# Performance work log

Hardware: AMD Instinct MI355X
Metric: run time of the kernel (lower is better)

The kernel has to match this reference:

```python
import jax, jax.numpy as jnp
import numpy as np

EMB = 128
HID = 4 * 32  # 4*hidden_dim = 128
N_NODES = 100000
N_EDGES = 800000


def setup_inputs() -> dict:
    key = jax.random.key(0)
    k1, k2, k3, k4 = jax.random.split(key, 4)
    node_emb = jax.random.normal(k1, (N_NODES, EMB), dtype=jnp.float32)
    edge_index = jax.random.randint(k2, (2, N_EDGES), 0, N_NODES, dtype=jnp.int64)
    # xavier_uniform for Linear weights, zeros bias; LayerNorm gamma=1, beta=0
    lim1 = float(np.sqrt(6.0 / (2 * EMB + HID)))
    W1 = jax.random.uniform(k3, (2 * EMB, HID), minval=-lim1, maxval=lim1, dtype=jnp.float32)
    b1 = jnp.zeros((HID,), dtype=jnp.float32)
    ln_g = jnp.ones((HID,), dtype=jnp.float32)
    ln_b = jnp.zeros((HID,), dtype=jnp.float32)
    lim2 = float(np.sqrt(6.0 / (HID + 1)))
    W2 = jax.random.uniform(k4, (HID, 1), minval=-lim2, maxval=lim2, dtype=jnp.float32)
    b2 = jnp.zeros((1,), dtype=jnp.float32)
    return {"node_emb": node_emb, "edge_index": edge_index,
            "W1": W1, "b1": b1, "ln_g": ln_g, "ln_b": ln_b, "W2": W2, "b2": b2}


def reference(node_emb, edge_index, W1, b1, ln_g, ln_b, W2, b2):
    src, dst = edge_index[0], edge_index[1]
    # gather + concat: [E, 2*EMB]
    edge_emb = jnp.concatenate([node_emb[src], node_emb[dst]], axis=1)
    h = edge_emb @ W1 + b1  # [E, HID]
    # LayerNorm over last dim (eps=1e-5, torch default)
    mu = jnp.mean(h, axis=-1, keepdims=True)
    var = jnp.var(h, axis=-1, keepdims=True)
    h = (h - mu) * jax.lax.rsqrt(var + 1e-5) * ln_g + ln_b
    h = jax.nn.relu(h)  # Dropout is identity in eval mode
    w = jax.nn.sigmoid(h @ W2 + b2)  # [E, 1]
    w = jnp.nan_to_num(w, nan=0.5)
    return w
```

## Files before the change

### kernel.cpp

```cpp
#include <hip/hip_runtime.h>
#include <hip/hip_bf16.h>
#include <math.h>

#define EMB 128
#define HID 128
#define NCOL 256

typedef __attribute__((ext_vector_type(8))) short short8v;
typedef __attribute__((ext_vector_type(4))) float f32x4;

__device__ __forceinline__ unsigned short f2bf(float f) {
    union { float f; unsigned int u; } v; v.f = f;
    unsigned int r = (v.u + 0x7FFFu + ((v.u >> 16) & 1u)) >> 16;
    return (unsigned short)r;
}
__device__ __forceinline__ float bf2f(unsigned int u16) {
    return __uint_as_float(u16 << 16);
}

template<int CTRL>
__device__ __forceinline__ float dpp_add(float x) {
    int y = __builtin_amdgcn_update_dpp(0, __float_as_int(x), CTRL, 0xf, 0xf, true);
    return x + __int_as_float(y);
}
__device__ __forceinline__ float red16(float x) {
    x = dpp_add<0xB1>(x);
    x = dpp_add<0x4E>(x);
    x = dpp_add<0x141>(x);
    x = dpp_add<0x140>(x);
    return x;
}

__global__ __launch_bounds__(256) void w_prep(
    const float* __restrict__ W1, unsigned short* __restrict__ Wt)
{
    int idx = blockIdx.x * 256 + threadIdx.x;
    int c = idx >> 7;
    int k = idx & 127;
    float v = W1[(size_t)(k + ((c >> 7) << 7)) * HID + (c & 127)];
    Wt[idx] = f2bf(v);
}

__global__ __launch_bounds__(256) void proj_mfma(
    const float* __restrict__ A,
    const unsigned short* __restrict__ Wt,
    const float* __restrict__ b1,
    unsigned short* __restrict__ P,
    int N, int nTiles)
{
    const int w    = threadIdx.x >> 6;
    const int lane = threadIdx.x & 63;
    const int l16  = lane & 15;
    const int lk   = lane >> 4;

    short8v afrag[4][4];
#pragma unroll
    for (int cf = 0; cf < 4; ++cf)
#pragma unroll
        for (int ks = 0; ks < 4; ++ks) {
            int c = 64 * w + 16 * cf + l16;
            afrag[cf][ks] = *(const short8v*)(Wt + (size_t)c * EMB + 32 * ks + 8 * lk);
        }

    float4 b1v[4];
#pragma unroll
    for (int cf = 0; cf < 4; ++cf) {
        if (w < 2) b1v[cf] = *(const float4*)(b1 + 64 * w + 16 * cf + 4 * lk);
        else       b1v[cf] = make_float4(0.f, 0.f, 0.f, 0.f);
    }

    int t = blockIdx.x;
    if (t >= nTiles) return;

    float4 fbuf[8];
    {
        int node = t * 16 + l16;
        int nc   = node < N ? node : N - 1;
        const float* ap = A + (size_t)nc * EMB + 8 * lk;
#pragma unroll
        for (int ks = 0; ks < 4; ++ks) {
            fbuf[2 * ks]     = *(const float4*)(ap + 32 * ks);
            fbuf[2 * ks + 1] = *(const float4*)(ap + 32 * ks + 4);
        }
    }

    for (; t < nTiles; t += gridDim.x) {
        short8v bf[4];
#pragma unroll
        for (int ks = 0; ks < 4; ++ks) {
            float4 a0 = fbuf[2 * ks], a1 = fbuf[2 * ks + 1];
            short8v f = { (short)f2bf(a0.x), (short)f2bf(a0.y), (short)f2bf(a0.z), (short)f2bf(a0.w),
                          (short)f2bf(a1.x), (short)f2bf(a1.y), (short)f2bf(a1.z), (short)f2bf(a1.w) };
            bf[ks] = f;
        }

        int tn = t + gridDim.x;
        if (tn < nTiles) {
            int node = tn * 16 + l16;
            int nc   = node < N ? node : N - 1;
            const float* ap = A + (size_t)nc * EMB + 8 * lk;
#pragma unroll
            for (int ks = 0; ks < 4; ++ks) {
                fbuf[2 * ks]     = *(const float4*)(ap + 32 * ks);
                fbuf[2 * ks + 1] = *(const float4*)(ap + 32 * ks + 4);
            }
        }

        f32x4 acc[4];
#pragma unroll
        for (int cf = 0; cf < 4; ++cf) acc[cf] = (f32x4)0.0f;

#pragma unroll
        for (int ks = 0; ks < 4; ++ks)
#pragma unroll
            for (int cf = 0; cf < 4; ++cf)
                acc[cf] = __builtin_amdgcn_mfma_f32_16x16x32_bf16(
                    afrag[cf][ks], bf[ks], acc[cf], 0, 0, 0);

        int node = t * 16 + l16;
        if (node < N) {
            unsigned short* prow = P + (size_t)node * NCOL;
#pragma unroll
            for (int cf = 0; cf < 4; ++cf) {
                float v0 = acc[cf][0] + b1v[cf].x;
                float v1 = acc[cf][1] + b1v[cf].y;
                float v2 = acc[cf][2] + b1v[cf].z;
                float v3 = acc[cf][3] + b1v[cf].w;
                unsigned int u0 = (unsigned int)f2bf(v0) | ((unsigned int)f2bf(v1) << 16);
                unsigned int u1 = (unsigned int)f2bf(v2) | ((unsigned int)f2bf(v3) << 16);
                *(uint2*)(prow + 64 * w + 16 * cf + 4 * lk) = make_uint2(u0, u1);
            }
        }
    }
}

__global__ __launch_bounds__(256) void edge_kernel(
    const unsigned short* __restrict__ P,
    const int* __restrict__ ei,
    const float* __restrict__ lng,
    const float* __restrict__ lnb,
    const float* __restrict__ W2,
    const float* __restrict__ b2,
    float* __restrict__ out, int E)
{
    const int l16 = threadIdx.x & 15;
    const int c0  = l16 * 8;

    float vg[8], vbt[8], vw2[8];
#pragma unroll
    for (int i = 0; i < 8; i += 4) {
        *(float4*)&vg[i]  = *(const float4*)(lng + c0 + i);
        *(float4*)&vbt[i] = *(const float4*)(lnb + c0 + i);
        *(float4*)&vw2[i] = *(const float4*)(W2  + c0 + i);
    }
    const float bias2 = b2[0];

    int slot   = blockIdx.x * (blockDim.x >> 4) + (threadIdx.x >> 4);
    int nslots = gridDim.x * (blockDim.x >> 4);

    for (int e = slot; e < E; e += nslots) {
        int src = ei[e];
        int dst = ei[E + e];
        uint4 us = *(const uint4*)(P + (size_t)src * NCOL + c0);
        uint4 ud = *(const uint4*)(P + (size_t)dst * NCOL + HID + c0);

        float h[8];
        {
            unsigned int uu[4] = {us.x, us.y, us.z, us.w};
            unsigned int dd[4] = {ud.x, ud.y, ud.z, ud.w};
#pragma unroll
            for (int j = 0; j < 4; ++j) {
                h[2 * j]     = bf2f(uu[j] & 0xFFFFu) + bf2f(dd[j] & 0xFFFFu);
                h[2 * j + 1] = __uint_as_float(uu[j] & 0xFFFF0000u) +
                               __uint_as_float(dd[j] & 0xFFFF0000u);
            }
        }
        float s = 0.0f, sq = 0.0f;
#pragma unroll
        for (int i = 0; i < 8; ++i) {
            s += h[i];
            sq = fmaf(h[i], h[i], sq);
        }
        s  = red16(s);
        sq = red16(sq);

        float mu  = s * (1.0f / HID);
        float var = sq * (1.0f / HID) - mu * mu;
        float r   = rsqrtf(var + 1e-5f);
        float nmr = -mu * r;

        float z = 0.0f;
#pragma unroll
        for (int i = 0; i < 8; ++i) {
            float t = fmaf(h[i], r, nmr);
            float y = fmaf(t, vg[i], vbt[i]);
            y = fmaxf(y, 0.0f);
            z = fmaf(y, vw2[i], z);
        }
        z = red16(z);

        if (l16 == 0) {
            float zz = z + bias2;
            float wv = 1.0f / (1.0f + expf(-zz));
            if (wv != wv) wv = 0.5f;
            out[e] = wv;
        }
    }
}

__global__ __launch_bounds__(256) void fused_kernel(
    const float* __restrict__ X,
    const int* __restrict__ ei,
    const float* __restrict__ W1,
    const float* __restrict__ b1,
    const float* __restrict__ lng,
    const float* __restrict__ lnb,
    const float* __restrict__ W2,
    const float* __restrict__ b2,
    float* __restrict__ out, int E)
{
    const int lane = threadIdx.x & 31;
    const int c0   = lane * 4;
    const float4 vb1 = *(const float4*)(b1  + c0);
    const float4 vg  = *(const float4*)(lng + c0);
    const float4 vbt = *(const float4*)(lnb + c0);
    const float4 vw2 = *(const float4*)(W2  + c0);
    const float bias2 = b2[0];

    int slot   = blockIdx.x * (blockDim.x >> 5) + (threadIdx.x >> 5);
    int nslots = gridDim.x * (blockDim.x >> 5);

    for (int e = slot; e < E; e += nslots) {
        int src = ei[e];
        int dst = ei[E + e];
        const float* xs = X + (size_t)src * EMB;
        const float* xd = X + (size_t)dst * EMB;
        float h0 = vb1.x, h1 = vb1.y, h2 = vb1.z, h3 = vb1.w;
        for (int k = 0; k < EMB; ++k) {
            float a  = xs[k];
            float4 w = *(const float4*)(W1 + (size_t)k * HID + c0);
            h0 = fmaf(a, w.x, h0); h1 = fmaf(a, w.y, h1);
            h2 = fmaf(a, w.z, h2); h3 = fmaf(a, w.w, h3);
        }
        for (int k = 0; k < EMB; ++k) {
            float a  = xd[k];
            float4 w = *(const float4*)(W1 + (size_t)(EMB + k) * HID + c0);
            h0 = fmaf(a, w.x, h0); h1 = fmaf(a, w.y, h1);
            h2 = fmaf(a, w.z, h2); h3 = fmaf(a, w.w, h3);
        }
        float s  = h0 + h1 + h2 + h3;
        float sq = h0 * h0 + h1 * h1 + h2 * h2 + h3 * h3;
#pragma unroll
        for (int m = 16; m >= 1; m >>= 1) {
            s  += __shfl_xor(s,  m, 32);
            sq += __shfl_xor(sq, m, 32);
        }
        float mu  = s * (1.0f / HID);
        float var = sq * (1.0f / HID) - mu * mu;
        float r   = rsqrtf(var + 1e-5f);
        float y0 = fmaxf(fmaf((h0 - mu) * r, vg.x, vbt.x), 0.0f);
        float y1 = fmaxf(fmaf((h1 - mu) * r, vg.y, vbt.y), 0.0f);
        float y2 = fmaxf(fmaf((h2 - mu) * r, vg.z, vbt.z), 0.0f);
        float y3 = fmaxf(fmaf((h3 - mu) * r, vg.w, vbt.w), 0.0f);
        float z = y0 * vw2.x + y1 * vw2.y + y2 * vw2.z + y3 * vw2.w;
#pragma unroll
        for (int m = 16; m >= 1; m >>= 1) z += __shfl_xor(z, m, 32);
        if (lane == 0) {
            float zz = z + bias2;
            float wv = 1.0f / (1.0f + expf(-zz));
            if (wv != wv) wv = 0.5f;
            out[e] = wv;
        }
    }
}

extern "C" void kernel_launch(void* const* d_in, const int* in_sizes, int n_in,
                              void* d_out, int out_size, void* d_ws, size_t ws_size,
                              hipStream_t stream) {
    const float* node_emb = (const float*)d_in[0];
    const int*   ei       = (const int*)d_in[1];
    const float* W1       = (const float*)d_in[2];
    const float* b1       = (const float*)d_in[3];
    const float* lng      = (const float*)d_in[4];
    const float* lnb      = (const float*)d_in[5];
    const float* W2       = (const float*)d_in[6];
    const float* b2       = (const float*)d_in[7];
    float* out = (float*)d_out;

    const int N = in_sizes[0] / EMB;
    const int E = in_sizes[1] / 2;

    const size_t pBytes = (size_t)N * NCOL * sizeof(unsigned short);
    const size_t need   = pBytes + (size_t)NCOL * EMB * sizeof(unsigned short);

    if (ws_size >= need) {
        unsigned short* P  = (unsigned short*)d_ws;
        unsigned short* Wt = (unsigned short*)((char*)d_ws + pBytes);

        w_prep<<<(NCOL * EMB) / 256, 256, 0, stream>>>(W1, Wt);

        int nTiles = (N + 15) / 16;
        int gridP  = nTiles < 2048 ? nTiles : 2048;
        proj_mfma<<<gridP, 256, 0, stream>>>(node_emb, Wt, b1, P, N, nTiles);

        edge_kernel<<<4096, 256, 0, stream>>>(P, ei, lng, lnb, W2, b2, out, E);
    } else {
        fused_kernel<<<2048, 256, 0, stream>>>(node_emb, ei, W1, b1, lng, lnb,
                                               W2, b2, out, E);
    }
}
```

Baseline: 198.0 us.

## Stage 64-node tiles in swizzled LDS as bf16 for projection MFMA

The node projection kernel now loads a 64-node tile per block cooperatively with coalesced float4 reads. It converts the values to bf16 and stores them in an XOR-swizzled shared memory buffer, which every wave then reads from to feed MFMA for all four 16-node groups. Before, each wave separately loaded the same 16 nodes from global memory and prefetched through a grid-stride loop. The change removes four-fold redundant global reads and the strided access pattern, at the cost of 16KB of LDS per block, a barrier, and no overlap between loads of one tile and compute on the next.

```diff
diff --git a/kernel.cpp b/kernel.cpp
--- a/kernel.cpp
+++ b/kernel.cpp
@@ -48,10 +48,18 @@
     unsigned short* __restrict__ P,
     int N, int nTiles)
 {
-    const int w    = threadIdx.x >> 6;
-    const int lane = threadIdx.x & 63;
+    __shared__ unsigned short lds_bf[64 * 128];
+    char* ldsb = (char*)lds_bf;
+
+    const int tid  = threadIdx.x;
+    const int w    = tid >> 6;
+    const int lane = tid & 63;
     const int l16  = lane & 15;
     const int lk   = lane >> 4;
+
+    const int t = blockIdx.x;
+    if (t >= nTiles) return;
+    const int n0 = t * 64;
 
     short8v afrag[4][4];
 #pragma unroll
@@ -69,55 +77,42 @@
         else       b1v[cf] = make_float4(0.f, 0.f, 0.f, 0.f);
     }
 
-    int t = blockIdx.x;
-    if (t >= nTiles) return;
-
-    float4 fbuf[8];
-    {
-        int node = t * 16 + l16;
-        int nc   = node < N ? node : N - 1;
-        const float* ap = A + (size_t)nc * EMB + 8 * lk;
+#pragma unroll
+    for (int i = 0; i < 8; ++i) {
+        int g   = tid + 256 * i;
+        int row = g >> 5;
+        int c4  = g & 31;
+        int nc  = n0 + row; nc = nc < N ? nc : N - 1;
+        float4 v = *(const float4*)(A + (size_t)nc * EMB + c4 * 4);
+        unsigned int u0 = (unsigned int)f2bf(v.x) | ((unsigned int)f2bf(v.y) << 16);
+        unsigned int u1 = (unsigned int)f2bf(v.z) | ((unsigned int)f2bf(v.w) << 16);
+        int byte = (row << 8) + (c4 << 3);
+        byte ^= (row & 7) << 4;
+        *(uint2*)(ldsb + byte) = make_uint2(u0, u1);
+    }
+    __syncthreads();
+
+#pragma unroll
+    for (int ng = 0; ng < 4; ++ng) {
+        int node_l = 16 * ng + l16;
+        short8v bfr[4];
 #pragma unroll
         for (int ks = 0; ks < 4; ++ks) {
-            fbuf[2 * ks]     = *(const float4*)(ap + 32 * ks);
-            fbuf[2 * ks + 1] = *(const float4*)(ap + 32 * ks + 4);
-        }
-    }
-
-    for (; t < nTiles; t += gridDim.x) {
-        short8v bf[4];
-#pragma unroll
-        for (int ks = 0; ks < 4; ++ks) {
-            float4 a0 = fbuf[2 * ks], a1 = fbuf[2 * ks + 1];
-            short8v f = { (short)f2bf(a0.x), (short)f2bf(a0.y), (short)f2bf(a0.z), (short)f2bf(a0.w),
-                          (short)f2bf(a1.x), (short)f2bf(a1.y), (short)f2bf(a1.z), (short)f2bf(a1.w) };
-            bf[ks] = f;
-        }
-
-        int tn = t + gridDim.x;
-        if (tn < nTiles) {
-            int node = tn * 16 + l16;
-            int nc   = node < N ? node : N - 1;
-            const float* ap = A + (size_t)nc * EMB + 8 * lk;
-#pragma unroll
-            for (int ks = 0; ks < 4; ++ks) {
-                fbuf[2 * ks]     = *(const float4*)(ap + 32 * ks);
-                fbuf[2 * ks + 1] = *(const float4*)(ap + 32 * ks + 4);
-            }
-        }
-
+            int byte = (node_l << 8) + ((32 * ks + 8 * lk) << 1);
+            byte ^= (node_l & 7) << 4;
+            bfr[ks] = *(const short8v*)(ldsb + byte);
+        }
         f32x4 acc[4];
 #pragma unroll
         for (int cf = 0; cf < 4; ++cf) acc[cf] = (f32x4)0.0f;
-
 #pragma unroll
         for (int ks = 0; ks < 4; ++ks)
 #pragma unroll
             for (int cf = 0; cf < 4; ++cf)
                 acc[cf] = __builtin_amdgcn_mfma_f32_16x16x32_bf16(
-                    afrag[cf][ks], bf[ks], acc[cf], 0, 0, 0);
-
-        int node = t * 16 + l16;
+                    afrag[cf][ks], bfr[ks], acc[cf], 0, 0, 0);
+
+        int node = n0 + node_l;
         if (node < N) {
             unsigned short* prow = P + (size_t)node * NCOL;
 #pragma unroll
@@ -299,9 +294,8 @@
 
         w_prep<<<(NCOL * EMB) / 256, 256, 0, stream>>>(W1, Wt);
 
-        int nTiles = (N + 15) / 16;
-        int gridP  = nTiles < 2048 ? nTiles : 2048;
-        proj_mfma<<<gridP, 256, 0, stream>>>(node_emb, Wt, b1, P, N, nTiles);
+        int nTiles = (N + 63) / 64;
+        proj_mfma<<<nTiles, 256, 0, stream>>>(node_emb, Wt, b1, P, N, nTiles);
 
         edge_kernel<<<4096, 256, 0, stream>>>(P, ei, lng, lnb, W2, b2, out, E);
     } else {
```

After: 183.0 us. -7.6%, faster.
